# Optimization experiments

Measured on AMD Instinct MI355X. Metric: run time of the kernel, lower is better.

The kernel has to match this reference:

```python
import jax, jax.numpy as jnp
import numpy as np

RADIUS = 0.2
NSAMPLE = 32
EPS = 1e-5
MLP = [128, 128, 256]


def setup_inputs() -> dict:
    key = jax.random.key(0)
    ks = jax.random.split(key, 8)
    B, N, D = 4, 4096, 64
    xyz = jax.random.uniform(ks[0], (B, N, 3), dtype=jnp.float32)  # unit cube
    points = jax.random.normal(ks[1], (B, N, D), dtype=jnp.float32)
    inp = {"xyz": xyz, "points": points}
    last = D + 3  # in_channel = 67
    for li, out in enumerate(MLP):
        kw, kb = jax.random.split(ks[2 + li])
        lim = 1.0 / np.sqrt(last)
        inp[f"w{li}"] = jax.random.uniform(kw, (out, last), jnp.float32, -lim, lim)
        inp[f"b{li}"] = jax.random.uniform(kb, (out,), jnp.float32, -lim, lim)
        inp[f"g{li}"] = jnp.ones((out,), jnp.float32)   # BN gamma
        inp[f"bt{li}"] = jnp.zeros((out,), jnp.float32)  # BN beta
        last = out
    return inp


def _query_ball(xyz):
    """Ball query: for each point, the NSAMPLE lowest-index neighbors within RADIUS.
    xyz: [B,N,3] -> group_idx [B,N,NSAMPLE] int32."""
    N = xyz.shape[1]
    sq = jnp.sum(xyz * xyz, axis=-1)  # [B,N]
    # squared pairwise distances [B,N,N]
    d = sq[:, :, None] + sq[:, None, :] - 2.0 * jnp.einsum('bnc,bmc->bnm', xyz, xyz)
    idx = jnp.where(d > RADIUS ** 2, N, jnp.arange(N, dtype=jnp.int32)[None, None, :])
    # smallest NSAMPLE indices == top_k of negated values (matches sort()[:, :, :k])
    neg, _ = jax.lax.top_k(-idx, NSAMPLE)
    gidx = -neg  # ascending
    # replace out-of-radius sentinel N with the first (closest-index) neighbor;
    # self-distance 0 <= r^2 guarantees gidx[...,0] < N
    gidx = jnp.where(gidx == N, gidx[:, :, :1], gidx)
    return gidx


def _bn(x, gamma, beta):
    """BatchNorm (training-mode batch stats) over all axes except channel axis 1."""
    axes = tuple(a for a in range(x.ndim) if a != 1)
    m = jnp.mean(x, axes, keepdims=True)
    v = jnp.mean(jnp.square(x - m), axes, keepdims=True)  # biased var, as torch BN
    shape = (1, -1) + (1,) * (x.ndim - 2)
    return (x - m) * jax.lax.rsqrt(v + EPS) * gamma.reshape(shape) + beta.reshape(shape)


def reference(xyz, points, w0, b0, g0, bt0, w1, b1, g1, bt1, w2, b2, g2, bt2):
    gidx = _query_ball(xyz)  # [B,N,ns]
    gather = jax.vmap(lambda a, i: a[i])  # per-batch gather
    gxyz = gather(xyz, gidx) - xyz[:, :, None, :]      # [B,N,ns,3] relative coords
    gpts = gather(points, gidx)                        # [B,N,ns,D]
    feat = jnp.concatenate([gxyz, gpts], axis=-1)      # [B,N,ns,3+D]
    x = jnp.transpose(feat, (0, 3, 2, 1))              # [B,C,ns,N]
    # layer 0: 1x1 Conv2d + BN2d + ReLU, then max-pool over neighbors
    x = jnp.einsum('bcsn,oc->bosn', x, w0) + b0[None, :, None, None]
    x = jax.nn.relu(_bn(x, g0, bt0))
    x = jnp.max(x, axis=2)                             # [B,C,N]
    # layer 1,2: 1x1 Conv1d + BN1d + ReLU
    x = jnp.einsum('bcn,oc->bon', x, w1) + b1[None, :, None]
    x = jax.nn.relu(_bn(x, g1, bt1))
    x = jnp.einsum('bcn,oc->bon', x, w2) + b2[None, :, None]
    x = jax.nn.relu(_bn(x, g2, bt2))
    return xyz, jnp.transpose(x, (0, 2, 1))            # (new_xyz [B,N,3], new_points [B,N,256])
```

## Files before the change

kernel.cpp:

```cpp
#include <hip/hip_runtime.h>
#include <hip/hip_bf16.h>

#define BN_EPS 1e-5f

typedef _Float16 half8 __attribute__((ext_vector_type(8)));
typedef _Float16 half4v __attribute__((ext_vector_type(4)));
typedef float f32x4v  __attribute__((ext_vector_type(4)));

static __device__ __forceinline__ float fmul(float a, float b){ return __fmul_rn(a,b); }
static __device__ __forceinline__ float fadd(float a, float b){ return __fadd_rn(a,b); }

#define NB0 16
#define NB1 16
#define NB2 8

__global__ __launch_bounds__(256) void prep_kernel(const float* __restrict__ xyz,
                                                   const float* __restrict__ pts,
                                                   const float* __restrict__ w0,
                                                   const float* __restrict__ w1,
                                                   const float* __restrict__ w2,
                                                   const float* __restrict__ b0,
                                                   _Float16* __restrict__ ypt,
                                                   _Float16* __restrict__ w1h,
                                                   _Float16* __restrict__ w2h,
                                                   float4* __restrict__ wcq,
                                                   float4* __restrict__ xyzw,
                                                   float* __restrict__ stats)
{
    __shared__ half8 FL[578];
    __shared__ half8 WfL[1024];
    __shared__ half8 W2L[136];

    const int t = threadIdx.x;
    const unsigned bid = blockIdx.x;

    if (bid < 256) {
        const int p0 = bid * 64;
        const int lane = t & 63, wv = t >> 6;
        const int wr = wv >> 1, wc = wv & 1;
        const int lm = lane & 15, lg = lane >> 4;
        const int i2 = (lg == 0) ? lm : 16;

        for (int idx = t; idx < 1024; idx += 256) {
            int rg = idx >> 7, rem = idx & 127;
            int kk = rem >> 6, l = rem & 63;
            int row = rg*16 + (l & 15);
            int k0  = kk*32 + ((l >> 4) << 3);
            half8 v;
            #pragma unroll
            for (int e = 0; e < 8; ++e)
                v[e] = (_Float16)w0[row*67 + k0 + e + 3];
            WfL[idx] = v;
        }
        for (int idx = t; idx < 128; idx += 256) {
            int tile = idx >> 4, l = idx & 15;
            half8 v = {};
            v[0] = (_Float16)w0[idx*67 + 0];
            v[1] = (_Float16)w0[idx*67 + 1];
            v[2] = (_Float16)w0[idx*67 + 2];
            W2L[tile*17 + l] = v;
        }
        if (t < 8) { half8 z = {}; W2L[t*17 + 16] = z; }

        for (int idx = t; idx < 512; idx += 256) {
            int pt = idx >> 3, grp = idx & 7;
            const float4* p4 = (const float4*)(pts + (size_t)(p0 + pt)*64 + grp*8);
            float4 a = p4[0], b4 = p4[1];
            half8 v;
            v[0]=(_Float16)a.x;  v[1]=(_Float16)a.y;  v[2]=(_Float16)a.z;  v[3]=(_Float16)a.w;
            v[4]=(_Float16)b4.x; v[5]=(_Float16)b4.y; v[6]=(_Float16)b4.z; v[7]=(_Float16)b4.w;
            FL[pt*9 + grp] = v;
        }
        if (t < 64) {
            const float* xg = xyz + (size_t)(p0 + t)*3;
            half8 v = {};
            v[0]=(_Float16)xg[0]; v[1]=(_Float16)xg[1]; v[2]=(_Float16)xg[2];
            FL[t*9 + 8] = v;
        }
        if (t == 64) { half8 z = {}; FL[576] = z; }
        __syncthreads();

        f32x4v acc[2][4];
        #pragma unroll
        for (int pi = 0; pi < 2; ++pi)
            #pragma unroll
            for (int ci = 0; ci < 4; ++ci)
                #pragma unroll
                for (int j = 0; j < 4; ++j) acc[pi][ci][j] = 0.f;

        #pragma unroll
        for (int kk = 0; kk < 2; ++kk) {
            half8 pf[2], wf[4];
            #pragma unroll
            for (int pi = 0; pi < 2; ++pi) pf[pi] = FL[(wr*32 + pi*16 + lm)*9 + kk*4 + lg];
            #pragma unroll
            for (int ci = 0; ci < 4; ++ci) wf[ci] = WfL[(4*wc + ci)*128 + kk*64 + lane];
            #pragma unroll
            for (int pi = 0; pi < 2; ++pi)
                #pragma unroll
                for (int ci = 0; ci < 4; ++ci)
                    acc[pi][ci] = __builtin_amdgcn_mfma_f32_16x16x32_f16(pf[pi], wf[ci], acc[pi][ci], 0, 0, 0);
        }
        {
            half8 pf[2], wf[4];
            #pragma unroll
            for (int pi = 0; pi < 2; ++pi)
                pf[pi] = FL[(lg == 0) ? ((wr*32 + pi*16 + lm)*9 + 8) : 576];
            #pragma unroll
            for (int ci = 0; ci < 4; ++ci) wf[ci] = W2L[(4*wc + ci)*17 + i2];
            #pragma unroll
            for (int pi = 0; pi < 2; ++pi)
                #pragma unroll
                for (int ci = 0; ci < 4; ++ci)
                    acc[pi][ci] = __builtin_amdgcn_mfma_f32_16x16x32_f16(pf[pi], wf[ci], acc[pi][ci], 0, 0, 0);
        }

        #pragma unroll
        for (int pi = 0; pi < 2; ++pi) {
            #pragma unroll
            for (int j = 0; j < 4; ++j) {
                int n = p0 + wr*32 + pi*16 + lg*4 + j;
                size_t basep = (size_t)n * 128;
                #pragma unroll
                for (int ci = 0; ci < 4; ++ci)
                    ypt[basep + wc*64 + ci*16 + lm] = (_Float16)acc[pi][ci][j];
            }
        }
        return;
    }
    if (bid < 260) {
        int wb = bid - 256;
        if (wb == 0) {
            for (int i = t; i < 4096; i += 256) {
                float4 v = ((const float4*)w1)[i];
                half4v h;
                h[0]=(_Float16)v.x; h[1]=(_Float16)v.y; h[2]=(_Float16)v.z; h[3]=(_Float16)v.w;
                ((half4v*)w1h)[i] = h;
            }
        } else if (wb <= 2) {
            int i0 = (wb - 1) * 4096;
            for (int i = t; i < 4096; i += 256) {
                float4 v = ((const float4*)w2)[i0 + i];
                half4v h;
                h[0]=(_Float16)v.x; h[1]=(_Float16)v.y; h[2]=(_Float16)v.z; h[3]=(_Float16)v.w;
                ((half4v*)w2h)[i0 + i] = h;
            }
        } else {
            for (int idx = t; idx < 128; idx += 256) {
                _Float16 h0 = (_Float16)w0[idx*67 + 0];
                _Float16 h1 = (_Float16)w0[idx*67 + 1];
                _Float16 h2 = (_Float16)w0[idx*67 + 2];
                wcq[idx] = make_float4((float)h0, (float)h1, (float)h2, b0[idx]);
            }
            for (int i = t; i < 12288; i += 256) stats[i] = 0.f;
        }
        return;
    }
    {
        const int p0 = (bid - 260) * 1024;
        for (int k = 0; k < 4; ++k) {
            int pt = p0 + k*256 + t;
            const float* xp = xyz + (size_t)pt * 3;
            float x = xp[0], y = xp[1], z = xp[2];
            float sq = fadd(fadd(fmul(x,x), fmul(y,y)), fmul(z,z));
            xyzw[pt] = make_float4(x, y, z, sq);
        }
    }
}

__global__ __launch_bounds__(256) void bqpool_kernel(const float4* __restrict__ xyzw,
                                                     const _Float16* __restrict__ ypt,
                                                     const float4* __restrict__ wcq,
                                                     const float* __restrict__ xyz,
                                                     float* __restrict__ s0a,
                                                     float* __restrict__ q0a,
                                                     _Float16* __restrict__ xm,
                                                     float* __restrict__ outbase)
{
    __shared__ int   idxs[4][32];
    __shared__ float psh[2][4][128];

    const int t = threadIdx.x;
    const unsigned bid = blockIdx.x;
    if (bid >= 4096) {
        int i = (bid - 4096) * 256 + t;
        ((float4*)outbase)[i] = ((const float4*)xyz)[i];
        return;
    }
    const int lane = t & 63;
    const int wv   = t >> 6;
    const int q = bid * 4 + wv;
    const int b = q >> 12;
    const int n = q & 4095;
    const float4* xw = xyzw + (size_t)b * 4096;
    const float4 qf = xw[n];

    int count = 0;
    int first = -1;
    for (int cbase = 0; cbase < 4096 && count < 32; cbase += 1024) {
        float4 rv[16];
        #pragma unroll
        for (int i = 0; i < 16; ++i) rv[i] = xw[cbase + i*64 + lane];
        #pragma unroll
        for (int i = 0; i < 16; ++i) {
            const float4 mf = rv[i];
            const float e = fadd(fadd(fmul(qf.x,mf.x), fmul(qf.y,mf.y)), fmul(qf.z,mf.z));
            const float d = __fsub_rn(fadd(qf.w, mf.w), fmul(2.0f, e));
            const bool in = !(d > 0.04f);
            const unsigned long long mask = __ballot(in);
            if (in) {
                int pos = count + __popcll(mask & ((1ull << lane) - 1ull));
                if (pos < 32) idxs[wv][pos] = cbase + i*64 + lane;
            }
            if (first < 0 && mask) first = cbase + i*64 + __ffsll((unsigned long long)mask) - 1;
            count += __popcll(mask);
        }
    }
    if (count < 32) {
        int slot = count + lane;
        if (slot < 32) idxs[wv][slot] = first;
    }
    __syncthreads();

    const int li = lane & 31, hw = lane >> 5;
    const half4v* Y4 = (const half4v*)ypt;
    const float4 wq0 = wcq[li*4+0], wq1 = wcq[li*4+1], wq2 = wcq[li*4+2], wq3 = wcq[li*4+3];
    const float x0 = qf.x, x1 = qf.y, x2 = qf.z;
    float cc[4];
    cc[0] = wq0.w - (wq0.x*x0 + wq0.y*x1 + wq0.z*x2);
    cc[1] = wq1.w - (wq1.x*x0 + wq1.y*x1 + wq1.z*x2);
    cc[2] = wq2.w - (wq2.x*x0 + wq2.y*x1 + wq2.z*x2);
    cc[3] = wq3.w - (wq3.x*x0 + wq3.y*x1 + wq3.z*x2);
    const int rbase = (q >> 12) << 12;

    float m[4]  = {-3.4e38f,-3.4e38f,-3.4e38f,-3.4e38f};
    float sy[4] = {0.f,0.f,0.f,0.f};
    float yy[4] = {0.f,0.f,0.f,0.f};
    #pragma unroll
    for (int i = 0; i < 16; ++i) {
        int g = idxs[wv][2*i + hw];
        half4v h = Y4[(size_t)(rbase + g)*32 + li];
        #pragma unroll
        for (int k = 0; k < 4; ++k) {
            float y = (float)h[k];
            m[k]  = fmaxf(m[k], y);
            sy[k] += y;
            yy[k] = fmaf(y, y, yy[k]);
        }
    }
    #pragma unroll
    for (int k = 0; k < 4; ++k) {
        m[k]   = fmaxf(m[k], __shfl_xor(m[k], 32));
        sy[k] += __shfl_xor(sy[k], 32);
        yy[k] += __shfl_xor(yy[k], 32);
    }
    if (hw == 0) {
        half4v ov;
        ov[0] = (_Float16)(m[0] + cc[0]);
        ov[1] = (_Float16)(m[1] + cc[1]);
        ov[2] = (_Float16)(m[2] + cc[2]);
        ov[3] = (_Float16)(m[3] + cc[3]);
        ((half4v*)xm)[(size_t)q*32 + li] = ov;
        #pragma unroll
        for (int k = 0; k < 4; ++k) {
            psh[0][wv][li*4 + k] = sy[k] + 32.f*cc[k];
            psh[1][wv][li*4 + k] = yy[k] + 2.f*cc[k]*sy[k] + 32.f*cc[k]*cc[k];
        }
    }
    __syncthreads();
    if (t < 128) {
        const int bank = bid & (NB0 - 1);
        float s  = psh[0][0][t] + psh[0][1][t] + psh[0][2][t] + psh[0][3][t];
        float qv = psh[1][0][t] + psh[1][1][t] + psh[1][2][t] + psh[1][3][t];
        atomicAdd(&s0a[bank*128 + t], s);
        atomicAdd(&q0a[bank*128 + t], qv);
    }
}

template<int OC, int NBOUT>
__global__ __launch_bounds__(256) void conv12_mfma_kernel(
    const _Float16* __restrict__ x, const _Float16* __restrict__ wh, const float* __restrict__ bias,
    const float* __restrict__ inS, const float* __restrict__ inQ,
    const float* __restrict__ gamma, const float* __restrict__ beta, float invc,
    _Float16* __restrict__ y, float* __restrict__ outS, float* __restrict__ outQ)
{
    __shared__ half8 Wf[8][4][64];
    __shared__ half8 Xf[4][4][64];
    __shared__ float scs[128], shs[128];
    __shared__ float psh[2][2][2][64];

    const int t = threadIdx.x, lane = t & 63, wv = t >> 6;
    const int wr = wv >> 1, wc = wv & 1;
    const int lm = lane & 15, lg = lane >> 4;
    const int n0 = blockIdx.x * 64;
    const int rb = blockIdx.y * 128;
    const int b  = blockIdx.z;

    if (t < 128) {
        float s = 0.f, q = 0.f;
        #pragma unroll
        for (int k = 0; k < NB0; ++k) { s += inS[k*128 + t]; q += inQ[k*128 + t]; }
        float m = s * invc;
        float v = q * invc - m*m;
        float scale = gamma[t] * rsqrtf(v + BN_EPS);
        scs[t] = scale;
        shs[t] = beta[t] - m * scale;
    }
    __syncthreads();

    for (int idx = t; idx < 8*4*64; idx += 256) {
        int rg = idx >> 8, rem = idx & 255;
        int kk = rem >> 6, l = rem & 63;
        int row = rb + rg*16 + (l & 15);
        int k0  = kk*32 + (l >> 4)*8;
        Wf[rg][kk][l] = *(const half8*)(wh + row*128 + k0);
    }
    for (int idx = t; idx < 4*4*64; idx += 256) {
        int ng = idx >> 8, rem = idx & 255;
        int kk = rem >> 6, l = rem & 63;
        int n  = n0 + ng*16 + (l & 15);
        int c0 = kk*32 + (l >> 4)*8;
        half8 xv = *(const half8*)(x + (((size_t)((b << 12) + n)) << 7) + c0);
        half8 v;
        #pragma unroll
        for (int e = 0; e < 8; ++e)
            v[e] = (_Float16)fmaxf(fmaf((float)xv[e], scs[c0+e], shs[c0+e]), 0.f);
        Xf[ng][kk][l] = v;
    }
    __syncthreads();

    f32x4v acc[2][4];
    #pragma unroll
    for (int ci = 0; ci < 4; ++ci) {
        float bvv = bias[rb + wc*64 + ci*16 + lm];
        #pragma unroll
        for (int pi = 0; pi < 2; ++pi)
            #pragma unroll
            for (int j = 0; j < 4; ++j) acc[pi][ci][j] = bvv;
    }
    #pragma unroll
    for (int kk = 0; kk < 4; ++kk) {
        half8 pf[2], wf[4];
        #pragma unroll
        for (int pi = 0; pi < 2; ++pi) pf[pi] = Xf[2*wr + pi][kk][lane];
        #pragma unroll
        for (int ci = 0; ci < 4; ++ci) wf[ci] = Wf[4*wc + ci][kk][lane];
        #pragma unroll
        for (int pi = 0; pi < 2; ++pi)
            #pragma unroll
            for (int ci = 0; ci < 4; ++ci)
                acc[pi][ci] = __builtin_amdgcn_mfma_f32_16x16x32_f16(pf[pi], wf[ci], acc[pi][ci], 0, 0, 0);
    }

    float ssum[4], ssq[4];
    #pragma unroll
    for (int ci = 0; ci < 4; ++ci) { ssum[ci] = 0.f; ssq[ci] = 0.f; }
    #pragma unroll
    for (int pi = 0; pi < 2; ++pi) {
        #pragma unroll
        for (int j = 0; j < 4; ++j) {
            int n = n0 + wr*32 + pi*16 + lg*4 + j;
            size_t basep = (size_t)((b << 12) + n) * OC + rb;
            #pragma unroll
            for (int ci = 0; ci < 4; ++ci) {
                float v = acc[pi][ci][j];
                y[basep + wc*64 + ci*16 + lm] = (_Float16)v;
                ssum[ci] += v;
                ssq[ci]  = fmaf(v, v, ssq[ci]);
            }
        }
    }
    #pragma unroll
    for (int ci = 0; ci < 4; ++ci) {
        float s  = ssum[ci], s2 = ssq[ci];
        s  += __shfl_xor(s, 16);  s  += __shfl_xor(s, 32);
        s2 += __shfl_xor(s2, 16); s2 += __shfl_xor(s2, 32);
        if (lg == 0) {
            psh[0][wr][wc][ci*16 + lm] = s;
            psh[1][wr][wc][ci*16 + lm] = s2;
        }
    }
    __syncthreads();
    if (t < 128) {
        const int bank = (blockIdx.x + blockIdx.y + (blockIdx.z << 2)) & (NBOUT - 1);
        atomicAdd(&outS[(size_t)bank*OC + rb + t], psh[0][0][t >> 6][t & 63] + psh[0][1][t >> 6][t & 63]);
        atomicAdd(&outQ[(size_t)bank*OC + rb + t], psh[1][0][t >> 6][t & 63] + psh[1][1][t >> 6][t & 63]);
    }
}

__global__ __launch_bounds__(256) void final_apply_kernel(const _Float16* __restrict__ y2h,
                                                          const float* __restrict__ s2a,
                                                          const float* __restrict__ q2a,
                                                          const float* __restrict__ gamma,
                                                          const float* __restrict__ beta,
                                                          float invc,
                                                          float* __restrict__ outbase)
{
    __shared__ float scs[256], shs[256];
    const int t = threadIdx.x;
    {
        float s = 0.f, q = 0.f;
        #pragma unroll
        for (int k = 0; k < NB2; ++k) { s += s2a[k*256 + t]; q += q2a[k*256 + t]; }
        float m = s * invc;
        float v = q * invc - m*m;
        float scale = gamma[t] * rsqrtf(v + BN_EPS);
        scs[t] = scale;
        shs[t] = beta[t] - m * scale;
    }
    __syncthreads();
    int i = blockIdx.x * 256 + t;
    half8 v = ((const half8*)y2h)[i];
    int c0 = (i & 31) * 8;
    float4 o0, o1;
    o0.x = fmaxf(fmaf((float)v[0], scs[c0+0], shs[c0+0]), 0.f);
    o0.y = fmaxf(fmaf((float)v[1], scs[c0+1], shs[c0+1]), 0.f);
    o0.z = fmaxf(fmaf((float)v[2], scs[c0+2], shs[c0+2]), 0.f);
    o0.w = fmaxf(fmaf((float)v[3], scs[c0+3], shs[c0+3]), 0.f);
    o1.x = fmaxf(fmaf((float)v[4], scs[c0+4], shs[c0+4]), 0.f);
    o1.y = fmaxf(fmaf((float)v[5], scs[c0+5], shs[c0+5]), 0.f);
    o1.z = fmaxf(fmaf((float)v[6], scs[c0+6], shs[c0+6]), 0.f);
    o1.w = fmaxf(fmaf((float)v[7], scs[c0+7], shs[c0+7]), 0.f);
    float4* op = (float4*)(outbase + 49152);
    op[2*i]   = o0;
    op[2*i+1] = o1;
}

extern "C" void kernel_launch(void* const* d_in, const int* in_sizes, int n_in,
                              void* d_out, int out_size, void* d_ws, size_t ws_size,
                              hipStream_t stream)
{
    const float* xyz = (const float*)d_in[0];
    const float* pts = (const float*)d_in[1];
    const float* w0  = (const float*)d_in[2];
    const float* b0  = (const float*)d_in[3];
    const float* g0  = (const float*)d_in[4];
    const float* bt0 = (const float*)d_in[5];
    const float* w1  = (const float*)d_in[6];
    const float* b1  = (const float*)d_in[7];
    const float* g1  = (const float*)d_in[8];
    const float* bt1 = (const float*)d_in[9];
    const float* w2  = (const float*)d_in[10];
    const float* b2  = (const float*)d_in[11];
    const float* g2  = (const float*)d_in[12];
    const float* bt2 = (const float*)d_in[13];
    float* out = (float*)d_out;

    char* ws = (char*)d_ws;
    float4*   xyzw = (float4*)(ws + 2097152);
    _Float16* xmh  = (_Float16*)(ws + 4718592);
    _Float16* y1h  = (_Float16*)(ws + 8912896);
    _Float16* y2h  = (_Float16*)(ws + 13107200);
    float*    stb  = (float*)(ws + 21495808);
    float *s0a = stb,        *q0a = stb + 2048;
    float *s1a = stb + 4096, *q1a = stb + 6144;
    float *s2a = stb + 8192, *q2a = stb + 10240;
    char*     wb   = ws + (24u << 20);
    float4*   wcq  = (float4*)(wb + 20480);
    _Float16* w1h  = (_Float16*)(wb + 32768);
    _Float16* w2h  = (_Float16*)(wb + 98304);
    _Float16* ypt  = (_Float16*)(ws + ((ws_size >= (38u << 20)) ? (size_t)(32u << 20)
                                                                : (size_t)13107200));

    prep_kernel<<<276, 256, 0, stream>>>(xyz, pts, w0, w1, w2, b0, ypt,
                                         w1h, w2h, wcq, xyzw, stb);
    bqpool_kernel<<<4144, 256, 0, stream>>>(xyzw, ypt, wcq, xyz, s0a, q0a, xmh, out);
    conv12_mfma_kernel<128, NB1><<<dim3(64,1,4), 256, 0, stream>>>(xmh, w1h, b1, s0a, q0a,
                                                                   g0, bt0, 1.f/524288.f,
                                                                   y1h, s1a, q1a);
    conv12_mfma_kernel<256, NB2><<<dim3(64,2,4), 256, 0, stream>>>(y1h, w2h, b2, s1a, q1a,
                                                                   g1, bt1, 1.f/16384.f,
                                                                   y2h, s2a, q2a);
    final_apply_kernel<<<2048, 256, 0, stream>>>(y2h, s2a, q2a, g2, bt2, 1.f/16384.f, out);
}
```

Before: 71.69 us.

## Stage candidate xyz chunks in shared memory for ball query with 512-thread blocks

The ball-query kernel now uses 512-thread blocks covering 8 query points. Candidate point coordinates are loaded cooperatively into a double-buffered shared-memory tile, so the 8 waves share one set of global reads. Each wave previously read all candidates straight from global or L2. The change adds a block-wide barrier per 1024-point chunk, and waves can no longer leave early once they have 32 neighbours. It also uses 32KB of LDS per block, which may limit occupancy.

```diff
diff --git a/kernel.cpp b/kernel.cpp
--- a/kernel.cpp
+++ b/kernel.cpp
@@ -168,7 +168,7 @@
     }
 }
 
-__global__ __launch_bounds__(256) void bqpool_kernel(const float4* __restrict__ xyzw,
+__global__ __launch_bounds__(512) void bqpool_kernel(const float4* __restrict__ xyzw,
                                                      const _Float16* __restrict__ ypt,
                                                      const float4* __restrict__ wcq,
                                                      const float* __restrict__ xyz,
@@ -177,50 +177,64 @@
                                                      _Float16* __restrict__ xm,
                                                      float* __restrict__ outbase)
 {
-    __shared__ int   idxs[4][32];
-    __shared__ float psh[2][4][128];
+    __shared__ float4 ch[2][1024];
+    __shared__ int   idxs[8][32];
+    __shared__ float psh[2][8][128];
 
     const int t = threadIdx.x;
     const unsigned bid = blockIdx.x;
-    if (bid >= 4096) {
-        int i = (bid - 4096) * 256 + t;
+    if (bid >= 2048) {
+        int i = (bid - 2048) * 512 + t;
         ((float4*)outbase)[i] = ((const float4*)xyz)[i];
         return;
     }
     const int lane = t & 63;
     const int wv   = t >> 6;
-    const int q = bid * 4 + wv;
+    const int q = bid * 8 + wv;
     const int b = q >> 12;
     const int n = q & 4095;
     const float4* xw = xyzw + (size_t)b * 4096;
     const float4 qf = xw[n];
 
+    #pragma unroll
+    for (int i = 0; i < 2; ++i) ch[0][i*512 + t] = xw[i*512 + t];
+    __syncthreads();
+
     int count = 0;
     int first = -1;
-    for (int cbase = 0; cbase < 4096 && count < 32; cbase += 1024) {
-        float4 rv[16];
-        #pragma unroll
-        for (int i = 0; i < 16; ++i) rv[i] = xw[cbase + i*64 + lane];
-        #pragma unroll
-        for (int i = 0; i < 16; ++i) {
-            const float4 mf = rv[i];
-            const float e = fadd(fadd(fmul(qf.x,mf.x), fmul(qf.y,mf.y)), fmul(qf.z,mf.z));
-            const float d = __fsub_rn(fadd(qf.w, mf.w), fmul(2.0f, e));
-            const bool in = !(d > 0.04f);
-            const unsigned long long mask = __ballot(in);
-            if (in) {
-                int pos = count + __popcll(mask & ((1ull << lane) - 1ull));
-                if (pos < 32) idxs[wv][pos] = cbase + i*64 + lane;
-            }
-            if (first < 0 && mask) first = cbase + i*64 + __ffsll((unsigned long long)mask) - 1;
-            count += __popcll(mask);
-        }
+    for (int c = 0; c < 4; ++c) {
+        float4 pr[2];
+        if (c < 3) {
+            #pragma unroll
+            for (int i = 0; i < 2; ++i) pr[i] = xw[(c+1)*1024 + i*512 + t];
+        }
+        if (count < 32) {
+            const float4* cb = ch[c & 1];
+            #pragma unroll
+            for (int i = 0; i < 16; ++i) {
+                const float4 mf = cb[i*64 + lane];
+                const float e = fadd(fadd(fmul(qf.x,mf.x), fmul(qf.y,mf.y)), fmul(qf.z,mf.z));
+                const float d = __fsub_rn(fadd(qf.w, mf.w), fmul(2.0f, e));
+                const bool in = !(d > 0.04f);
+                const unsigned long long mask = __ballot(in);
+                if (in) {
+                    int pos = count + __popcll(mask & ((1ull << lane) - 1ull));
+                    if (pos < 32) idxs[wv][pos] = c*1024 + i*64 + lane;
+                }
+                if (first < 0 && mask) first = c*1024 + i*64 + __ffsll((unsigned long long)mask) - 1;
+                count += __popcll(mask);
+            }
+        }
+        if (c < 3) {
+            #pragma unroll
+            for (int i = 0; i < 2; ++i) ch[(c+1) & 1][i*512 + t] = pr[i];
+        }
+        __syncthreads();
     }
     if (count < 32) {
         int slot = count + lane;
         if (slot < 32) idxs[wv][slot] = first;
     }
-    __syncthreads();
 
     const int li = lane & 31, hw = lane >> 5;
     const half4v* Y4 = (const half4v*)ypt;
@@ -270,8 +284,9 @@
     __syncthreads();
     if (t < 128) {
         const int bank = bid & (NB0 - 1);
-        float s  = psh[0][0][t] + psh[0][1][t] + psh[0][2][t] + psh[0][3][t];
-        float qv = psh[1][0][t] + psh[1][1][t] + psh[1][2][t] + psh[1][3][t];
+        float s = 0.f, qv = 0.f;
+        #pragma unroll
+        for (int w = 0; w < 8; ++w) { s += psh[0][w][t]; qv += psh[1][w][t]; }
         atomicAdd(&s0a[bank*128 + t], s);
         atomicAdd(&q0a[bank*128 + t], qv);
     }
@@ -464,7 +479,7 @@
 
     prep_kernel<<<276, 256, 0, stream>>>(xyz, pts, w0, w1, w2, b0, ypt,
                                          w1h, w2h, wcq, xyzw, stb);
-    bqpool_kernel<<<4144, 256, 0, stream>>>(xyzw, ypt, wcq, xyz, s0a, q0a, xmh, out);
+    bqpool_kernel<<<2072, 512, 0, stream>>>(xyzw, ypt, wcq, xyz, s0a, q0a, xmh, out);
     conv12_mfma_kernel<128, NB1><<<dim3(64,1,4), 256, 0, stream>>>(xmh, w1h, b1, s0a, q0a,
                                                                    g0, bt0, 1.f/524288.f,
                                                                    y1h, s1a, q1a);
```

New measurement: 75.21 us. 4.9% more time.

## Process four ball queries per wavefront to reuse candidate point loads

Applied to the files above, without the earlier changes.

Each wavefront now handles four query points instead of one. Every candidate xyz chunk loaded from memory is tested against all four queries, and the candidate scan uses smaller 256-point chunks with an early exit once all four queries have 32 neighbours. The grid shrinks about fourfold, and the per-block BN statistic atomics drop by the same factor. In exchange there are fewer waves to hide latency and more serial work per wave, and the barrier between writing and reading the per-wave index lists is removed.

```diff
diff --git a/kernel.cpp b/kernel.cpp
--- a/kernel.cpp
+++ b/kernel.cpp
@@ -177,94 +177,118 @@
                                                      _Float16* __restrict__ xm,
                                                      float* __restrict__ outbase)
 {
-    __shared__ int   idxs[4][32];
+    __shared__ int   idxs[16][32];
     __shared__ float psh[2][4][128];
 
     const int t = threadIdx.x;
     const unsigned bid = blockIdx.x;
-    if (bid >= 4096) {
-        int i = (bid - 4096) * 256 + t;
+    if (bid >= 1024) {
+        int i = (bid - 1024) * 256 + t;
         ((float4*)outbase)[i] = ((const float4*)xyz)[i];
         return;
     }
     const int lane = t & 63;
     const int wv   = t >> 6;
-    const int q = bid * 4 + wv;
-    const int b = q >> 12;
-    const int n = q & 4095;
+    const int q0 = bid * 16 + wv * 4;
+    const int b  = q0 >> 12;
     const float4* xw = xyzw + (size_t)b * 4096;
-    const float4 qf = xw[n];
-
-    int count = 0;
-    int first = -1;
-    for (int cbase = 0; cbase < 4096 && count < 32; cbase += 1024) {
-        float4 rv[16];
-        #pragma unroll
-        for (int i = 0; i < 16; ++i) rv[i] = xw[cbase + i*64 + lane];
-        #pragma unroll
-        for (int i = 0; i < 16; ++i) {
+
+    float4 qf[4];
+    #pragma unroll
+    for (int e = 0; e < 4; ++e) qf[e] = xw[(q0 + e) & 4095];
+
+    int cnt[4] = {0,0,0,0};
+    int fst[4] = {-1,-1,-1,-1};
+    for (int cb = 0; cb < 4096; cb += 256) {
+        float4 rv[4];
+        #pragma unroll
+        for (int i = 0; i < 4; ++i) rv[i] = xw[cb + i*64 + lane];
+        #pragma unroll
+        for (int i = 0; i < 4; ++i) {
             const float4 mf = rv[i];
-            const float e = fadd(fadd(fmul(qf.x,mf.x), fmul(qf.y,mf.y)), fmul(qf.z,mf.z));
-            const float d = __fsub_rn(fadd(qf.w, mf.w), fmul(2.0f, e));
-            const bool in = !(d > 0.04f);
-            const unsigned long long mask = __ballot(in);
-            if (in) {
-                int pos = count + __popcll(mask & ((1ull << lane) - 1ull));
-                if (pos < 32) idxs[wv][pos] = cbase + i*64 + lane;
-            }
-            if (first < 0 && mask) first = cbase + i*64 + __ffsll((unsigned long long)mask) - 1;
-            count += __popcll(mask);
-        }
-    }
-    if (count < 32) {
-        int slot = count + lane;
-        if (slot < 32) idxs[wv][slot] = first;
-    }
-    __syncthreads();
+            #pragma unroll
+            for (int e = 0; e < 4; ++e) {
+                if (cnt[e] < 32) {
+                    const float ee = fadd(fadd(fmul(qf[e].x,mf.x), fmul(qf[e].y,mf.y)), fmul(qf[e].z,mf.z));
+                    const float d  = __fsub_rn(fadd(qf[e].w, mf.w), fmul(2.0f, ee));
+                    const bool in = !(d > 0.04f);
+                    const unsigned long long mask = __ballot(in);
+                    if (in) {
+                        int pos = cnt[e] + __popcll(mask & ((1ull << lane) - 1ull));
+                        if (pos < 32) idxs[wv*4 + e][pos] = cb + i*64 + lane;
+                    }
+                    if (fst[e] < 0 && mask) fst[e] = cb + i*64 + __ffsll((unsigned long long)mask) - 1;
+                    cnt[e] += __popcll(mask);
+                }
+            }
+        }
+        if (cnt[0] >= 32 && cnt[1] >= 32 && cnt[2] >= 32 && cnt[3] >= 32) break;
+    }
+    #pragma unroll
+    for (int e = 0; e < 4; ++e) {
+        if (cnt[e] < 32) {
+            int slot = cnt[e] + lane;
+            if (slot < 32) idxs[wv*4 + e][slot] = fst[e];
+        }
+    }
 
     const int li = lane & 31, hw = lane >> 5;
     const half4v* Y4 = (const half4v*)ypt;
     const float4 wq0 = wcq[li*4+0], wq1 = wcq[li*4+1], wq2 = wcq[li*4+2], wq3 = wcq[li*4+3];
-    const float x0 = qf.x, x1 = qf.y, x2 = qf.z;
-    float cc[4];
-    cc[0] = wq0.w - (wq0.x*x0 + wq0.y*x1 + wq0.z*x2);
-    cc[1] = wq1.w - (wq1.x*x0 + wq1.y*x1 + wq1.z*x2);
-    cc[2] = wq2.w - (wq2.x*x0 + wq2.y*x1 + wq2.z*x2);
-    cc[3] = wq3.w - (wq3.x*x0 + wq3.y*x1 + wq3.z*x2);
-    const int rbase = (q >> 12) << 12;
-
-    float m[4]  = {-3.4e38f,-3.4e38f,-3.4e38f,-3.4e38f};
-    float sy[4] = {0.f,0.f,0.f,0.f};
-    float yy[4] = {0.f,0.f,0.f,0.f};
-    #pragma unroll
-    for (int i = 0; i < 16; ++i) {
-        int g = idxs[wv][2*i + hw];
-        half4v h = Y4[(size_t)(rbase + g)*32 + li];
+    const int rbase = (q0 >> 12) << 12;
+    float ss[4] = {0.f,0.f,0.f,0.f}, qq[4] = {0.f,0.f,0.f,0.f};
+
+    #pragma unroll
+    for (int e = 0; e < 4; ++e) {
+        const int q = q0 + e;
+        const float x0 = qf[e].x, x1 = qf[e].y, x2 = qf[e].z;
+        float cc[4];
+        cc[0] = wq0.w - (wq0.x*x0 + wq0.y*x1 + wq0.z*x2);
+        cc[1] = wq1.w - (wq1.x*x0 + wq1.y*x1 + wq1.z*x2);
+        cc[2] = wq2.w - (wq2.x*x0 + wq2.y*x1 + wq2.z*x2);
+        cc[3] = wq3.w - (wq3.x*x0 + wq3.y*x1 + wq3.z*x2);
+
+        float m[4]  = {-3.4e38f,-3.4e38f,-3.4e38f,-3.4e38f};
+        float sy[4] = {0.f,0.f,0.f,0.f};
+        float yy[4] = {0.f,0.f,0.f,0.f};
+        #pragma unroll
+        for (int i = 0; i < 16; ++i) {
+            int g = idxs[wv*4 + e][2*i + hw];
+            half4v h = Y4[(size_t)(rbase + g)*32 + li];
+            #pragma unroll
+            for (int k = 0; k < 4; ++k) {
+                float y = (float)h[k];
+                m[k]  = fmaxf(m[k], y);
+                sy[k] += y;
+                yy[k] = fmaf(y, y, yy[k]);
+            }
+        }
         #pragma unroll
         for (int k = 0; k < 4; ++k) {
-            float y = (float)h[k];
-            m[k]  = fmaxf(m[k], y);
-            sy[k] += y;
-            yy[k] = fmaf(y, y, yy[k]);
-        }
-    }
-    #pragma unroll
-    for (int k = 0; k < 4; ++k) {
-        m[k]   = fmaxf(m[k], __shfl_xor(m[k], 32));
-        sy[k] += __shfl_xor(sy[k], 32);
-        yy[k] += __shfl_xor(yy[k], 32);
-    }
+            m[k]   = fmaxf(m[k], __shfl_xor(m[k], 32));
+            sy[k] += __shfl_xor(sy[k], 32);
+            yy[k] += __shfl_xor(yy[k], 32);
+        }
+        if (hw == 0) {
+            half4v ov;
+            ov[0] = (_Float16)(m[0] + cc[0]);
+            ov[1] = (_Float16)(m[1] + cc[1]);
+            ov[2] = (_Float16)(m[2] + cc[2]);
+            ov[3] = (_Float16)(m[3] + cc[3]);
+            ((half4v*)xm)[(size_t)q*32 + li] = ov;
+        }
+        #pragma unroll
+        for (int k = 0; k < 4; ++k) {
+            ss[k] += sy[k] + 32.f*cc[k];
+            qq[k] += yy[k] + 2.f*cc[k]*sy[k] + 32.f*cc[k]*cc[k];
+        }
+    }
+
     if (hw == 0) {
-        half4v ov;
-        ov[0] = (_Float16)(m[0] + cc[0]);
-        ov[1] = (_Float16)(m[1] + cc[1]);
-        ov[2] = (_Float16)(m[2] + cc[2]);
-        ov[3] = (_Float16)(m[3] + cc[3]);
-        ((half4v*)xm)[(size_t)q*32 + li] = ov;
         #pragma unroll
         for (int k = 0; k < 4; ++k) {
-            psh[0][wv][li*4 + k] = sy[k] + 32.f*cc[k];
-            psh[1][wv][li*4 + k] = yy[k] + 2.f*cc[k]*sy[k] + 32.f*cc[k]*cc[k];
+            psh[0][wv][li*4 + k] = ss[k];
+            psh[1][wv][li*4 + k] = qq[k];
         }
     }
     __syncthreads();
@@ -464,7 +488,7 @@
 
     prep_kernel<<<276, 256, 0, stream>>>(xyz, pts, w0, w1, w2, b0, ypt,
                                          w1h, w2h, wcq, xyzw, stb);
-    bqpool_kernel<<<4144, 256, 0, stream>>>(xyzw, ypt, wcq, xyz, s0a, q0a, xmh, out);
+    bqpool_kernel<<<1072, 256, 0, stream>>>(xyzw, ypt, wcq, xyz, s0a, q0a, xmh, out);
     conv12_mfma_kernel<128, NB1><<<dim3(64,1,4), 256, 0, stream>>>(xmh, w1h, b1, s0a, q0a,
                                                                    g0, bt0, 1.f/524288.f,
                                                                    y1h, s1a, q1a);
```

Measured after the change: 76.16 us. 6.2% more time.

## Split ball-query candidate scan across waves and share ballot masks via LDS

Applied to the files above, without the earlier changes.

Each wave now scans a quarter of the 4096 candidates for all four queries in the block, writing ballot masks to shared memory. After a barrier, each wave compacts the first 32 in-radius indices from the 64 masks. This removes redundant candidate loads per wave and the sequential early-exit loop. The trade-off is that the early exit is lost, so every candidate is always tested for all four queries, and the kernel now depends on a block barrier.

```diff
diff --git a/kernel.cpp b/kernel.cpp
--- a/kernel.cpp
+++ b/kernel.cpp
@@ -177,6 +177,7 @@
                                                      _Float16* __restrict__ xm,
                                                      float* __restrict__ outbase)
 {
+    __shared__ unsigned long long mks[4][64];
     __shared__ int   idxs[4][32];
     __shared__ float psh[2][4][128];
 
@@ -189,49 +190,62 @@
     }
     const int lane = t & 63;
     const int wv   = t >> 6;
-    const int q = bid * 4 + wv;
-    const int b = q >> 12;
-    const int n = q & 4095;
+    const int q0 = bid * 4;
+    const int b  = q0 >> 12;
     const float4* xw = xyzw + (size_t)b * 4096;
-    const float4 qf = xw[n];
-
-    int count = 0;
-    int first = -1;
-    for (int cbase = 0; cbase < 4096 && count < 32; cbase += 1024) {
+
+    float4 qf[4];
+    #pragma unroll
+    for (int e = 0; e < 4; ++e) qf[e] = xw[(q0 + e) & 4095];
+
+    {
         float4 rv[16];
         #pragma unroll
-        for (int i = 0; i < 16; ++i) rv[i] = xw[cbase + i*64 + lane];
+        for (int i = 0; i < 16; ++i) rv[i] = xw[wv*1024 + i*64 + lane];
         #pragma unroll
         for (int i = 0; i < 16; ++i) {
             const float4 mf = rv[i];
-            const float e = fadd(fadd(fmul(qf.x,mf.x), fmul(qf.y,mf.y)), fmul(qf.z,mf.z));
-            const float d = __fsub_rn(fadd(qf.w, mf.w), fmul(2.0f, e));
-            const bool in = !(d > 0.04f);
-            const unsigned long long mask = __ballot(in);
-            if (in) {
-                int pos = count + __popcll(mask & ((1ull << lane) - 1ull));
-                if (pos < 32) idxs[wv][pos] = cbase + i*64 + lane;
-            }
-            if (first < 0 && mask) first = cbase + i*64 + __ffsll((unsigned long long)mask) - 1;
-            count += __popcll(mask);
-        }
-    }
-    if (count < 32) {
-        int slot = count + lane;
-        if (slot < 32) idxs[wv][slot] = first;
-    }
-    __syncthreads();
+            #pragma unroll
+            for (int e = 0; e < 4; ++e) {
+                const float ee = fadd(fadd(fmul(qf[e].x,mf.x), fmul(qf[e].y,mf.y)), fmul(qf[e].z,mf.z));
+                const float d  = __fsub_rn(fadd(qf[e].w, mf.w), fmul(2.0f, ee));
+                unsigned long long mk = __ballot(!(d > 0.04f));
+                if (lane == 0) mks[e][wv*16 + i] = mk;
+            }
+        }
+    }
+    __syncthreads();
+
+    int cnt = 0;
+    int fst = -1;
+    const unsigned long long lmask = (1ull << lane) - 1ull;
+    for (int r = 0; r < 64; ++r) {
+        if (cnt < 32) {
+            const unsigned long long mask = mks[wv][r];
+            if ((mask >> lane) & 1ull) {
+                int pos = cnt + __popcll(mask & lmask);
+                if (pos < 32) idxs[wv][pos] = r*64 + lane;
+            }
+            if (fst < 0 && mask) fst = r*64 + __ffsll((unsigned long long)mask) - 1;
+            cnt += __popcll(mask);
+        }
+    }
+    if (cnt < 32) {
+        int slot = cnt + lane;
+        if (slot < 32) idxs[wv][slot] = fst;
+    }
 
     const int li = lane & 31, hw = lane >> 5;
     const half4v* Y4 = (const half4v*)ypt;
     const float4 wq0 = wcq[li*4+0], wq1 = wcq[li*4+1], wq2 = wcq[li*4+2], wq3 = wcq[li*4+3];
-    const float x0 = qf.x, x1 = qf.y, x2 = qf.z;
+    const int rbase = (q0 >> 12) << 12;
+    const int q = q0 + wv;
+    const float x0 = qf[wv].x, x1 = qf[wv].y, x2 = qf[wv].z;
     float cc[4];
     cc[0] = wq0.w - (wq0.x*x0 + wq0.y*x1 + wq0.z*x2);
     cc[1] = wq1.w - (wq1.x*x0 + wq1.y*x1 + wq1.z*x2);
     cc[2] = wq2.w - (wq2.x*x0 + wq2.y*x1 + wq2.z*x2);
     cc[3] = wq3.w - (wq3.x*x0 + wq3.y*x1 + wq3.z*x2);
-    const int rbase = (q >> 12) << 12;
 
     float m[4]  = {-3.4e38f,-3.4e38f,-3.4e38f,-3.4e38f};
     float sy[4] = {0.f,0.f,0.f,0.f};
```

New measurement: 92.17 us. 1.29x slower.
